# Kernel tuning notes

Measured on AMD Instinct MI355X. Metric: run time of the kernel, lower is better.

Reference implementation:

```python
import jax, jax.numpy as jnp
import numpy as np

E, T, IN, OUT = 8, 16384, 1024, 1024  # n_groups, total_tokens, in_features, out_features


def setup_inputs() -> dict:
    key = jax.random.key(0)
    kx, kw, ks = jax.random.split(key, 3)
    x = jax.random.normal(kx, (T, IN), dtype=jnp.float32)
    # kaiming_uniform-ish scale for weight [E, OUT, IN]
    weight = jax.random.normal(kw, (E, OUT, IN), dtype=jnp.float32) * (1.0 / np.sqrt(IN))
    # ragged segment lengths that sum exactly to T (random cut points)
    cuts = jnp.sort(jax.random.randint(ks, (E - 1,), 0, T + 1)).astype(jnp.int32)
    seg_lens = jnp.diff(
        jnp.concatenate([jnp.zeros((1,), jnp.int32), cuts, jnp.full((1,), T, jnp.int32)])
    )
    return {"x": x, "weight": weight, "seg_lens": seg_lens}


def reference(x, weight, seg_lens):
    # Grouped GEMM: row t of x is multiplied by weight[g(t)].T where g(t) is the
    # segment (expert) that token t falls into per seg_lens. trans_b=True.
    n_groups = weight.shape[0]
    bounds = jnp.cumsum(seg_lens)                                  # [E]
    seg_id = jnp.searchsorted(bounds, jnp.arange(x.shape[0]), side="right")  # [T]
    y = jnp.zeros((x.shape[0], weight.shape[1]), dtype=x.dtype)
    for e in range(n_groups):  # small fixed loop over groups
        y = y + jnp.where((seg_id == e)[:, None], x @ weight[e].T, 0)
    return y
```

## Files before the change

kernel.cpp:

```cpp
#include <hip/hip_runtime.h>

#define T_TOK  16384
#define IN_F   1024
#define OUT_F  1024
#define NE     8

typedef __bf16 bf16;
typedef bf16  bf16x4 __attribute__((ext_vector_type(4)));
typedef bf16  bf16x8 __attribute__((ext_vector_type(8)));
typedef float f32x4  __attribute__((ext_vector_type(4)));

#define BM 256
#define BN 256
#define BK 64
#define GTHREADS 512
#define NBLOCKS 256
#define KCH (IN_F / BK)
#define SP_BLOCKS 112

#define CVT_THREADS 256
#define NX8 (T_TOK * IN_F / 8)
#define NW8 (NE * OUT_F * IN_F / 8)
#define NCVT8 (NX8 + NW8)

__global__ __launch_bounds__(CVT_THREADS)
void cvt_and_zero(const float* __restrict__ x, const float* __restrict__ w,
                  bf16* __restrict__ xb, bf16* __restrict__ wb,
                  const int* __restrict__ seg_lens, float* __restrict__ out)
{
    int r64 = T_TOK;
    {
        int slots = 0, start = 0;
        #pragma unroll
        for (int e = 0; e < NE; ++e) {
            int len = seg_lens[e];
            int nt  = (len + BM - 1) >> 8;
            if (slots <= 64 && slots + nt > 64) {
                r64 = start + (64 - slots) * BM;
            }
            slots += nt;
            start += len;
        }
    }
    const int zero8 = (T_TOK - r64) * (OUT_F / 8);
    const int zb8   = r64 * (OUT_F / 8);
    const int tot   = NCVT8 + zero8;

    for (int i = blockIdx.x * CVT_THREADS + threadIdx.x; i < tot;
         i += gridDim.x * CVT_THREADS) {
        if (i < NCVT8) {
            const bool isx = (i < NX8);
            const int  j   = isx ? i : i - NX8;
            f32x4 v0 = isx ? ((const f32x4*)x)[2*j]   : ((const f32x4*)w)[2*j];
            f32x4 v1 = isx ? ((const f32x4*)x)[2*j+1] : ((const f32x4*)w)[2*j+1];
            bf16x8 h;
            #pragma unroll
            for (int k = 0; k < 4; ++k) { h[k] = (bf16)v0[k]; h[4+k] = (bf16)v1[k]; }
            if (isx) ((bf16x8*)xb)[j] = h;
            else     ((bf16x8*)wb)[j] = h;
        } else {
            f32x4 z = {0.f, 0.f, 0.f, 0.f};
            const int j = zb8 + (i - NCVT8);
            ((f32x4*)out)[2*j]   = z;
            ((f32x4*)out)[2*j+1] = z;
        }
    }
}

__device__ __forceinline__ void gld_lds16(const bf16* g, bf16* l) {
    __builtin_amdgcn_global_load_lds(
        (const __attribute__((address_space(1))) void*)g,
        (__attribute__((address_space(3))) void*)l,
        16, 0, 0);
}

__device__ __forceinline__ void resolve_slot(const int* sl, int slot,
                                             int& e_sel, int& row0, int& rows)
{
    e_sel = -1; row0 = 0; rows = 0;
    int start = 0, acct = 0;
    #pragma unroll
    for (int e = 0; e < NE; ++e) {
        int len = sl[e];
        int nt  = (len + BM - 1) >> 8;
        if (e_sel < 0 && slot >= acct && slot < acct + nt) {
            e_sel = e;
            row0  = start + (slot - acct) * BM;
            int rm = start + len - row0;
            rows = rm < BM ? rm : BM;
        }
        acct  += nt;
        start += len;
    }
}

__device__ __forceinline__ void mfma_step(const bf16* __restrict__ Ab,
                                          const bf16* __restrict__ Bb,
                                          f32x4 (&acc)[8][4],
                                          int wr, int wc, int l16, int quad,
                                          int swz8)
{
    #pragma unroll
    for (int kk = 0; kk < 2; ++kk) {
        const int ce = (kk * 32 + quad * 8) ^ swz8;
        bf16x8 af[8], bfr[4];
        #pragma unroll
        for (int t = 0; t < 8; ++t)
            af[t] = *(const bf16x8*)(Ab + (wr * 128 + t * 16 + l16) * BK + ce);
        #pragma unroll
        for (int v = 0; v < 4; ++v)
            bfr[v] = *(const bf16x8*)(Bb + (wc * 64 + v * 16 + l16) * BK + ce);
        #pragma unroll
        for (int t = 0; t < 8; ++t)
            #pragma unroll
            for (int v = 0; v < 4; ++v)
                acc[t][v] = __builtin_amdgcn_mfma_f32_16x16x32_bf16(
                    af[t], bfr[v], acc[t][v], 0, 0, 0);
    }
}

__global__ __launch_bounds__(GTHREADS)
void grouped_gemm_main(const bf16* __restrict__ xb,
                       const bf16* __restrict__ wb,
                       const int*  __restrict__ seg_lens,
                       float* __restrict__ out)
{
    __shared__ __align__(16) bf16 As[2][BM * BK];
    __shared__ __align__(16) bf16 Bs[2][BN * BK];

    const int tile = blockIdx.x;
    const int slot = tile >> 2;
    const int col0 = (tile & 3) << 8;

    int sl[NE];
    #pragma unroll
    for (int e = 0; e < NE; ++e) sl[e] = seg_lens[e];

    int e_sel, row0, rows;
    resolve_slot(sl, slot, e_sel, row0, rows);
    if (e_sel < 0) return;

    const int tid  = threadIdx.x;
    const int lane = tid & 63;
    const int wave = tid >> 6;
    const int wr   = wave >> 2;
    const int wc   = wave & 3;
    const int quad = lane >> 4;
    const int l16  = lane & 15;
    const int rq   = lane >> 3;
    const int q0   = wave * 4;
    const int swz8 = (l16 & 7) * 8;

    const int ke_s = (((lane & 7) ^ rq) * 8);

    const bf16* wbase = wb + ((size_t)e_sel * OUT_F + (size_t)col0) * IN_F;

    const bf16* ga[4];
    const bf16* gb[4];
    #pragma unroll
    for (int i = 0; i < 4; ++i) {
        int q  = wave * 4 + i;
        int ra = row0 + q * 8 + rq;
        if (ra > T_TOK - 1) ra = T_TOK - 1;
        ga[i] = xb + (size_t)ra * IN_F + ke_s;
        gb[i] = wbase + (size_t)(q * 8 + rq) * IN_F + ke_s;
    }

    f32x4 acc[8][4] = {};

    #pragma unroll
    for (int i = 0; i < 4; ++i) {
        gld_lds16(ga[i], &As[0][(q0 + i) * 512]);
        gld_lds16(gb[i], &Bs[0][(q0 + i) * 512]);
    }

    for (int n = 0; n < KCH - 1; ++n) {
        const int kn  = (n + 1) * BK;
        const int nxt = (n + 1) & 1;
        #pragma unroll
        for (int i = 0; i < 4; ++i) {
            gld_lds16(ga[i] + kn, &As[nxt][(q0 + i) * 512]);
            gld_lds16(gb[i] + kn, &Bs[nxt][(q0 + i) * 512]);
        }
        asm volatile("s_waitcnt vmcnt(8)" ::: "memory");
        __builtin_amdgcn_s_barrier();
        __builtin_amdgcn_sched_barrier(0);
        mfma_step(&As[n & 1][0], &Bs[n & 1][0], acc, wr, wc, l16, quad, swz8);
        __builtin_amdgcn_sched_barrier(0);
        __builtin_amdgcn_s_barrier();
    }
    asm volatile("s_waitcnt vmcnt(0)" ::: "memory");
    __builtin_amdgcn_s_barrier();
    __builtin_amdgcn_sched_barrier(0);
    mfma_step(&As[(KCH - 1) & 1][0], &Bs[(KCH - 1) & 1][0], acc,
              wr, wc, l16, quad, swz8);

    #pragma unroll
    for (int t = 0; t < 8; ++t) {
        #pragma unroll
        for (int r = 0; r < 4; ++r) {
            int row = wr * 128 + t * 16 + quad * 4 + r;
            if (row < rows) {
                size_t ob = (size_t)(row0 + row) * OUT_F + col0 + wc * 64;
                #pragma unroll
                for (int v = 0; v < 4; ++v)
                    out[ob + v * 16 + l16] = acc[t][v][r];
            }
        }
    }
}

__global__ __launch_bounds__(GTHREADS)
void grouped_gemm_surplus(const bf16* __restrict__ xb,
                          const bf16* __restrict__ wb,
                          const int*  __restrict__ seg_lens,
                          float* __restrict__ out)
{
    __shared__ __align__(16) bf16 As[2][BM * BK];
    __shared__ __align__(16) bf16 Bs[2][BN * BK];

    const int tile   = NBLOCKS + (blockIdx.x >> 2);
    const int kslice = blockIdx.x & 3;

    int sl[NE];
    #pragma unroll
    for (int e = 0; e < NE; ++e) sl[e] = seg_lens[e];

    int n_slots = 0;
    #pragma unroll
    for (int e = 0; e < NE; ++e) n_slots += (sl[e] + BM - 1) >> 8;
    const int L = n_slots * (OUT_F / BN);
    if (tile >= L) return;

    const int slot = tile >> 2;
    const int col0 = (tile & 3) << 8;
    int e_sel, row0, rows;
    resolve_slot(sl, slot, e_sel, row0, rows);

    const int tid  = threadIdx.x;
    const int lane = tid & 63;
    const int wave = tid >> 6;
    const int wr   = wave >> 2;
    const int wc   = wave & 3;
    const int quad = lane >> 4;
    const int l16  = lane & 15;
    const int rq   = lane >> 3;
    const int ke   = (lane & 7) * 8;
    const int q0   = wave * 4;

    const bf16* wbase = wb + ((size_t)e_sel * OUT_F + (size_t)col0) * IN_F;

    const bf16* ga[4];
    const bf16* gb[4];
    #pragma unroll
    for (int i = 0; i < 4; ++i) {
        int q  = wave * 4 + i;
        int ra = row0 + q * 8 + rq;
        if (ra > T_TOK - 1) ra = T_TOK - 1;
        ga[i] = xb + (size_t)ra * IN_F + ke;
        gb[i] = wbase + (size_t)(q * 8 + rq) * IN_F + ke;
    }

    f32x4 acc[8][4] = {};

    const int kb0 = kslice * 4 * BK;

    #pragma unroll
    for (int i = 0; i < 4; ++i) {
        gld_lds16(ga[i] + kb0, &As[0][(q0 + i) * 512]);
        gld_lds16(gb[i] + kb0, &Bs[0][(q0 + i) * 512]);
    }
    __syncthreads();

    #pragma unroll
    for (int j = 0; j < 4; ++j) {
        const int cur = j & 1;
        if (j < 3) {
            const int kn = kb0 + (j + 1) * BK;
            #pragma unroll
            for (int i = 0; i < 4; ++i) {
                gld_lds16(ga[i] + kn, &As[cur ^ 1][(q0 + i) * 512]);
                gld_lds16(gb[i] + kn, &Bs[cur ^ 1][(q0 + i) * 512]);
            }
        }

        #pragma unroll
        for (int kk = 0; kk < 2; ++kk) {
            bf16x8 af[8], bfr[4];
            #pragma unroll
            for (int t = 0; t < 8; ++t)
                af[t] = *(const bf16x8*)(
                    &As[cur][(wr * 128 + t * 16 + l16) * BK + kk * 32 + quad * 8]);
            #pragma unroll
            for (int v = 0; v < 4; ++v)
                bfr[v] = *(const bf16x8*)(
                    &Bs[cur][(wc * 64 + v * 16 + l16) * BK + kk * 32 + quad * 8]);
            #pragma unroll
            for (int t = 0; t < 8; ++t)
                #pragma unroll
                for (int v = 0; v < 4; ++v)
                    acc[t][v] = __builtin_amdgcn_mfma_f32_16x16x32_bf16(
                        af[t], bfr[v], acc[t][v], 0, 0, 0);
        }

        __syncthreads();
    }

    #pragma unroll
    for (int t = 0; t < 8; ++t) {
        #pragma unroll
        for (int r = 0; r < 4; ++r) {
            int row = wr * 128 + t * 16 + quad * 4 + r;
            if (row < rows) {
                size_t ob = (size_t)(row0 + row) * OUT_F + col0 + wc * 64;
                #pragma unroll
                for (int v = 0; v < 4; ++v)
                    unsafeAtomicAdd(&out[ob + v * 16 + l16], acc[t][v][r]);
            }
        }
    }
}

#define FBM 128
#define FBK 32
#define FTHREADS 256
#define FROW_SLOTS 136

__global__ __launch_bounds__(FTHREADS)
void grouped_gemm_f32io_bf16(const float* __restrict__ x,
                             const float* __restrict__ wgt,
                             const int*  __restrict__ seg_lens,
                             float* __restrict__ out)
{
    __shared__ __align__(16) bf16 Asf[FBM * FBK];
    __shared__ __align__(16) bf16 Bsf[FBM * FBK];

    const int m    = blockIdx.y;
    const int col0 = blockIdx.x * FBM;

    int e_sel = -1, row0 = 0, rows = 0;
    {
        int start = 0, acct = 0;
        #pragma unroll
        for (int e = 0; e < NE; ++e) {
            int len = seg_lens[e];
            int nt  = (len + FBM - 1) >> 7;
            if (e_sel < 0 && m >= acct && m < acct + nt) {
                e_sel = e;
                row0  = start + (m - acct) * FBM;
                int rem = start + len - row0;
                rows = rem < FBM ? rem : FBM;
            }
            acct  += nt;
            start += len;
        }
    }
    if (e_sel < 0) return;

    const int tid  = threadIdx.x;
    const int lane = tid & 63;
    const int wave = tid >> 6;
    const int wm   = (wave >> 1) * 64;
    const int wn   = (wave & 1) * 64;
    const int quad = lane >> 4;
    const int l16  = lane & 15;

    const float* wbase = wgt + ((size_t)e_sel * OUT_F + (size_t)col0) * IN_F;

    f32x4 acc[4][4] = {};

    for (int k0 = 0; k0 < IN_F; k0 += FBK) {
        f32x4 a_st[4], b_st[4];
        #pragma unroll
        for (int t = 0; t < 4; ++t) {
            int c  = t * FTHREADS + tid;
            int rg = row0 + (c >> 3);
            if (rg > T_TOK - 1) rg = T_TOK - 1;
            a_st[t] = *(const f32x4*)(x + (size_t)rg * IN_F + k0 + (c & 7) * 4);
            b_st[t] = *(const f32x4*)(wbase + (size_t)(c >> 3) * IN_F + k0 + (c & 7) * 4);
        }

        __syncthreads();

        #pragma unroll
        for (int t = 0; t < 4; ++t) {
            int c = t * FTHREADS + tid;
            bf16x4 ha, hb;
            #pragma unroll
            for (int j = 0; j < 4; ++j) { ha[j] = (bf16)a_st[t][j]; hb[j] = (bf16)b_st[t][j]; }
            *(bf16x4*)(&Asf[(c >> 3) * FBK + (c & 7) * 4]) = ha;
            *(bf16x4*)(&Bsf[(c >> 3) * FBK + (c & 7) * 4]) = hb;
        }
        __syncthreads();

        bf16x8 af[4], bfr[4];
        #pragma unroll
        for (int t = 0; t < 4; ++t)
            af[t] = *(const bf16x8*)(&Asf[(wm + t * 16 + l16) * FBK + quad * 8]);
        #pragma unroll
        for (int v = 0; v < 4; ++v)
            bfr[v] = *(const bf16x8*)(&Bsf[(wn + v * 16 + l16) * FBK + quad * 8]);

        #pragma unroll
        for (int t = 0; t < 4; ++t)
            #pragma unroll
            for (int v = 0; v < 4; ++v)
                acc[t][v] = __builtin_amdgcn_mfma_f32_16x16x32_bf16(
                    af[t], bfr[v], acc[t][v], 0, 0, 0);
    }

    #pragma unroll
    for (int t = 0; t < 4; ++t) {
        #pragma unroll
        for (int r = 0; r < 4; ++r) {
            int row = wm + t * 16 + quad * 4 + r;
            if (row < rows) {
                size_t ob = (size_t)(row0 + row) * OUT_F + col0;
                #pragma unroll
                for (int v = 0; v < 4; ++v)
                    out[ob + wn + v * 16 + l16] = acc[t][v][r];
            }
        }
    }
}

extern "C" void kernel_launch(void* const* d_in, const int* in_sizes, int n_in,
                              void* d_out, int out_size, void* d_ws, size_t ws_size,
                              hipStream_t stream) {
    const float* x   = (const float*)d_in[0];
    const float* wgt = (const float*)d_in[1];
    const int*   seg = (const int*)d_in[2];
    float* out = (float*)d_out;

    const size_t xbytes = (size_t)T_TOK * IN_F * sizeof(bf16);
    const size_t wbytes = (size_t)NE * OUT_F * IN_F * sizeof(bf16);

    if (ws_size >= xbytes + wbytes) {
        bf16* xb = (bf16*)d_ws;
        bf16* wb = (bf16*)((char*)d_ws + xbytes);
        cvt_and_zero<<<dim3(2048, 1, 1), dim3(CVT_THREADS, 1, 1), 0, stream>>>(
            x, wgt, xb, wb, seg, out);
        grouped_gemm_main<<<dim3(NBLOCKS, 1, 1), dim3(GTHREADS, 1, 1), 0, stream>>>(
            xb, wb, seg, out);
        grouped_gemm_surplus<<<dim3(SP_BLOCKS, 1, 1), dim3(GTHREADS, 1, 1), 0, stream>>>(
            xb, wb, seg, out);
    } else {
        grouped_gemm_f32io_bf16<<<dim3(OUT_F / FBM, FROW_SLOTS, 1),
                                  dim3(FTHREADS, 1, 1), 0, stream>>>(x, wgt, seg, out);
    }
}
```

Measured before the change: 205.5 us.

## Interleave prefetch with quarter-step MFMA phases and remap tiles for XCD locality

Splits each K-chunk into four phases. Each phase issues one slice of the next chunk's global-to-LDS loads, reads a smaller set of fragments from LDS, and runs a 16-MFMA burst at raised wave priority, with barriers between phases. The aim is to spread memory traffic across the compute and cut register pressure from holding all fragments at once. It also remaps blockIdx so that consecutive tiles land on the same XCD, which should improve L2 reuse. The cost is many more barriers per K-chunk and waits with fewer loads in flight.

```diff
diff --git a/kernel.cpp b/kernel.cpp
--- a/kernel.cpp
+++ b/kernel.cpp
@@ -94,31 +94,6 @@
     }
 }
 
-__device__ __forceinline__ void mfma_step(const bf16* __restrict__ Ab,
-                                          const bf16* __restrict__ Bb,
-                                          f32x4 (&acc)[8][4],
-                                          int wr, int wc, int l16, int quad,
-                                          int swz8)
-{
-    #pragma unroll
-    for (int kk = 0; kk < 2; ++kk) {
-        const int ce = (kk * 32 + quad * 8) ^ swz8;
-        bf16x8 af[8], bfr[4];
-        #pragma unroll
-        for (int t = 0; t < 8; ++t)
-            af[t] = *(const bf16x8*)(Ab + (wr * 128 + t * 16 + l16) * BK + ce);
-        #pragma unroll
-        for (int v = 0; v < 4; ++v)
-            bfr[v] = *(const bf16x8*)(Bb + (wc * 64 + v * 16 + l16) * BK + ce);
-        #pragma unroll
-        for (int t = 0; t < 8; ++t)
-            #pragma unroll
-            for (int v = 0; v < 4; ++v)
-                acc[t][v] = __builtin_amdgcn_mfma_f32_16x16x32_bf16(
-                    af[t], bfr[v], acc[t][v], 0, 0, 0);
-    }
-}
-
 __global__ __launch_bounds__(GTHREADS)
 void grouped_gemm_main(const bf16* __restrict__ xb,
                        const bf16* __restrict__ wb,
@@ -128,7 +103,8 @@
     __shared__ __align__(16) bf16 As[2][BM * BK];
     __shared__ __align__(16) bf16 Bs[2][BN * BK];
 
-    const int tile = blockIdx.x;
+    const int b    = blockIdx.x;
+    const int tile = ((b & 7) << 5) | (b >> 3);
     const int slot = tile >> 2;
     const int col0 = (tile & 3) << 8;
 
@@ -174,26 +150,107 @@
         gld_lds16(gb[i], &Bs[0][(q0 + i) * 512]);
     }
 
-    for (int n = 0; n < KCH - 1; ++n) {
-        const int kn  = (n + 1) * BK;
-        const int nxt = (n + 1) & 1;
-        #pragma unroll
-        for (int i = 0; i < 4; ++i) {
-            gld_lds16(ga[i] + kn, &As[nxt][(q0 + i) * 512]);
-            gld_lds16(gb[i] + kn, &Bs[nxt][(q0 + i) * 512]);
-        }
-        asm volatile("s_waitcnt vmcnt(8)" ::: "memory");
-        __builtin_amdgcn_s_barrier();
+    for (int n = 0; n < KCH; ++n) {
+        const int  cur = n & 1;
+        const int  nxt = cur ^ 1;
+        const int  kn  = (n + 1) * BK;
+        const bool pf  = (n + 1 < KCH);
+        const bf16* Ab = &As[cur][0];
+        const bf16* Bb = &Bs[cur][0];
+        bf16x8 af[4], bfr[4];
+
+        if (pf) { gld_lds16(ga[0] + kn, &As[nxt][(q0 + 0) * 512]);
+                  gld_lds16(gb[0] + kn, &Bs[nxt][(q0 + 0) * 512]); }
+        if (pf) asm volatile("s_waitcnt vmcnt(2)" ::: "memory");
+        else    asm volatile("s_waitcnt vmcnt(0)" ::: "memory");
+        __builtin_amdgcn_s_barrier();
+        {
+            const int ce = (quad * 8) ^ swz8;
+            #pragma unroll
+            for (int v = 0; v < 4; ++v)
+                bfr[v] = *(const bf16x8*)(Bb + (wc * 64 + v * 16 + l16) * BK + ce);
+            #pragma unroll
+            for (int t = 0; t < 4; ++t)
+                af[t] = *(const bf16x8*)(Ab + (wr * 128 + t * 16 + l16) * BK + ce);
+        }
+        asm volatile("s_waitcnt lgkmcnt(0)" ::: "memory");
         __builtin_amdgcn_sched_barrier(0);
-        mfma_step(&As[n & 1][0], &Bs[n & 1][0], acc, wr, wc, l16, quad, swz8);
+        __builtin_amdgcn_s_setprio(1);
+        #pragma unroll
+        for (int t = 0; t < 4; ++t)
+            #pragma unroll
+            for (int v = 0; v < 4; ++v)
+                acc[t][v] = __builtin_amdgcn_mfma_f32_16x16x32_bf16(
+                    af[t], bfr[v], acc[t][v], 0, 0, 0);
+        __builtin_amdgcn_s_setprio(0);
+        __builtin_amdgcn_s_barrier();
+
+        if (pf) { gld_lds16(ga[1] + kn, &As[nxt][(q0 + 1) * 512]);
+                  gld_lds16(gb[1] + kn, &Bs[nxt][(q0 + 1) * 512]); }
+        {
+            const int ce = (quad * 8) ^ swz8;
+            #pragma unroll
+            for (int t = 0; t < 4; ++t)
+                af[t] = *(const bf16x8*)(Ab + (wr * 128 + 64 + t * 16 + l16) * BK + ce);
+        }
+        __builtin_amdgcn_s_barrier();
+        asm volatile("s_waitcnt lgkmcnt(0)" ::: "memory");
         __builtin_amdgcn_sched_barrier(0);
-        __builtin_amdgcn_s_barrier();
-    }
-    asm volatile("s_waitcnt vmcnt(0)" ::: "memory");
-    __builtin_amdgcn_s_barrier();
-    __builtin_amdgcn_sched_barrier(0);
-    mfma_step(&As[(KCH - 1) & 1][0], &Bs[(KCH - 1) & 1][0], acc,
-              wr, wc, l16, quad, swz8);
+        __builtin_amdgcn_s_setprio(1);
+        #pragma unroll
+        for (int t = 0; t < 4; ++t)
+            #pragma unroll
+            for (int v = 0; v < 4; ++v)
+                acc[4 + t][v] = __builtin_amdgcn_mfma_f32_16x16x32_bf16(
+                    af[t], bfr[v], acc[4 + t][v], 0, 0, 0);
+        __builtin_amdgcn_s_setprio(0);
+        __builtin_amdgcn_s_barrier();
+
+        if (pf) { gld_lds16(ga[2] + kn, &As[nxt][(q0 + 2) * 512]);
+                  gld_lds16(gb[2] + kn, &Bs[nxt][(q0 + 2) * 512]); }
+        {
+            const int ce = (32 + quad * 8) ^ swz8;
+            #pragma unroll
+            for (int v = 0; v < 4; ++v)
+                bfr[v] = *(const bf16x8*)(Bb + (wc * 64 + v * 16 + l16) * BK + ce);
+            #pragma unroll
+            for (int t = 0; t < 4; ++t)
+                af[t] = *(const bf16x8*)(Ab + (wr * 128 + t * 16 + l16) * BK + ce);
+        }
+        __builtin_amdgcn_s_barrier();
+        asm volatile("s_waitcnt lgkmcnt(0)" ::: "memory");
+        __builtin_amdgcn_sched_barrier(0);
+        __builtin_amdgcn_s_setprio(1);
+        #pragma unroll
+        for (int t = 0; t < 4; ++t)
+            #pragma unroll
+            for (int v = 0; v < 4; ++v)
+                acc[t][v] = __builtin_amdgcn_mfma_f32_16x16x32_bf16(
+                    af[t], bfr[v], acc[t][v], 0, 0, 0);
+        __builtin_amdgcn_s_setprio(0);
+        __builtin_amdgcn_s_barrier();
+
+        if (pf) { gld_lds16(ga[3] + kn, &As[nxt][(q0 + 3) * 512]);
+                  gld_lds16(gb[3] + kn, &Bs[nxt][(q0 + 3) * 512]); }
+        {
+            const int ce = (32 + quad * 8) ^ swz8;
+            #pragma unroll
+            for (int t = 0; t < 4; ++t)
+                af[t] = *(const bf16x8*)(Ab + (wr * 128 + 64 + t * 16 + l16) * BK + ce);
+        }
+        __builtin_amdgcn_s_barrier();
+        asm volatile("s_waitcnt lgkmcnt(0)" ::: "memory");
+        __builtin_amdgcn_sched_barrier(0);
+        __builtin_amdgcn_s_setprio(1);
+        #pragma unroll
+        for (int t = 0; t < 4; ++t)
+            #pragma unroll
+            for (int v = 0; v < 4; ++v)
+                acc[4 + t][v] = __builtin_amdgcn_mfma_f32_16x16x32_bf16(
+                    af[t], bfr[v], acc[4 + t][v], 0, 0, 0);
+        __builtin_amdgcn_s_setprio(0);
+        __builtin_amdgcn_s_barrier();
+    }
 
     #pragma unroll
     for (int t = 0; t < 8; ++t) {
```

After: 215.4 us. 4.8% more time.
